# Optimization experiments

Hardware: AMD Instinct MI355X
Metric: run time of the kernel (lower is better)

## Reference

```python
import jax, jax.numpy as jnp
import numpy as np

HID = 128
OUT = 128
NC = 100000
NA = 1024
FC = 256
FA = 4096

def _sage(x_src, x_dst, ei, Wl, bl, Wr):
    # PyG SAGEConv, mean aggregation, bipartite:
    # out[i] = lin_l(mean_{j->i} x_src[j]) + lin_r(x_dst[i])
    n_dst = x_dst.shape[0]
    src, dst = ei[0], ei[1]
    msg = x_src[src]                                  # [E, F_src] gather
    agg = jax.ops.segment_sum(msg, dst, num_segments=n_dst)
    cnt = jax.ops.segment_sum(jnp.ones((ei.shape[1],), x_src.dtype), dst, num_segments=n_dst)
    mean = agg / jnp.clip(cnt, 1.0, None)[:, None]
    return mean @ Wl.T + bl + x_dst @ Wr.T

def setup_inputs() -> dict:
    key = jax.random.key(0)
    ks = jax.random.split(key, 20)
    d = {}
    d["article_x"] = jax.random.normal(ks[0], (1, FA), jnp.float32)
    d["community_x"] = jax.random.normal(ks[1], (NC, FC), jnp.float32)
    # bipartite edges: row = article node idx (<NA), col = community idx (<NC)
    d["e_wb"] = jnp.stack([jax.random.randint(ks[2], (500000,), 0, NA, jnp.int32),
                            jax.random.randint(ks[3], (500000,), 0, NC, jnp.int32)])
    d["e_mb"] = jnp.stack([jax.random.randint(ks[4], (500000,), 0, NA, jnp.int32),
                            jax.random.randint(ks[5], (500000,), 0, NC, jnp.int32)])
    d["e_cc"] = jax.random.randint(ks[6], (2, 800000), 0, NC, jnp.int32)
    s = lambda k, sh: jax.random.normal(k, sh, jnp.float32) * (1.0 / np.sqrt(sh[-1]))
    d["W_lin1"] = s(ks[7], (NA, FA)); d["b_lin1"] = jnp.zeros((NA,), jnp.float32)
    d["Wl1"] = s(ks[8], (HID, 1));   d["bl1"] = jnp.zeros((HID,), jnp.float32); d["Wr1"] = s(ks[9], (HID, FC))
    d["Wl2"] = s(ks[10], (HID, 1));  d["bl2"] = jnp.zeros((HID,), jnp.float32); d["Wr2"] = s(ks[11], (HID, HID))
    d["Wl3"] = s(ks[12], (HID, HID)); d["bl3"] = jnp.zeros((HID,), jnp.float32); d["Wr3"] = s(ks[13], (HID, FC))
    d["W_lin2"] = s(ks[14], (OUT, HID)); d["b_lin2"] = jnp.zeros((OUT,), jnp.float32)
    d["Wd1"] = s(ks[15], (OUT, 2 * OUT)); d["bd1"] = jnp.zeros((OUT,), jnp.float32)
    d["Wd2"] = s(ks[16], (1, OUT)); d["bd2"] = jnp.zeros((1,), jnp.float32)
    return d

def reference(article_x, community_x, e_wb, e_mb, e_cc,
              W_lin1, b_lin1, Wl1, bl1, Wr1, Wl2, bl2, Wr2,
              Wl3, bl3, Wr3, W_lin2, b_lin2, Wd1, bd1, Wd2, bd2):
    # encoder
    art = (article_x @ W_lin1.T + b_lin1).reshape(NA, 1)      # [1024, 1]
    h1 = jax.nn.relu(_sage(art, community_x, e_wb, Wl1, bl1, Wr1))   # [NC, HID]
    h2 = jax.nn.relu(_sage(art, h1, e_mb, Wl2, bl2, Wr2))            # [NC, HID]
    h3 = jax.nn.relu(_sage(h2, community_x, e_cc, Wl3, bl3, Wr3))    # [NC, HID]
    z = h3 @ W_lin2.T + b_lin2                                       # [NC, OUT]
    # edge decoder on interacts_with edges
    row, col = e_cc[0], e_cc[1]
    zz = jnp.concatenate([z[row], z[col]], axis=-1)                  # [E, 2*OUT]
    h = jax.nn.relu(zz @ Wd1.T + bd1)
    return (h @ Wd2.T + bd2).reshape(-1)                             # [E]
```

## Files before the change

kernel.cpp:

```cpp
#include <hip/hip_runtime.h>

#define NC 100000
#define NA 1024
#define FA 4096
#define NREP 8

typedef _Float16 half8 __attribute__((ext_vector_type(8)));
typedef _Float16 half4v __attribute__((ext_vector_type(4)));
typedef _Float16 half2v __attribute__((ext_vector_type(2)));
typedef float floatx4 __attribute__((ext_vector_type(4)));

#define CNT_OFF 4294967296.0
#define CNT_INV 2.3283064365386963e-10

__device__ __forceinline__ void cvt_range(const float* __restrict__ in,
                                          _Float16* __restrict__ out, int n4,
                                          int bid, int nb) {
    int t = bid * 256 + threadIdx.x;
    int stride = nb * 256;
    for (int i = t; i < n4; i += stride) {
        float4 v = ((const float4*)in)[i];
        half4v h = {(_Float16)v.x, (_Float16)v.y, (_Float16)v.z, (_Float16)v.w};
        ((half4v*)out)[i] = h;
    }
}

__device__ __forceinline__ void edge_seg(const int* __restrict__ ei, int E,
                                         const float* __restrict__ art,
                                         double* __restrict__ acd, int bid, int nb) {
    int t = bid * 256 + threadIdx.x;
    int stride = nb * 256;
    for (int e = t; e < E; e += stride) {
        int s = ei[e], d = ei[E + e];
        atomicAdd(&acd[d], (double)art[s] + CNT_OFF);
    }
}

__device__ __forceinline__ void hist_seg(const int* __restrict__ ei, int E,
                                         int* __restrict__ deg, int bid, int nb) {
    int t = bid * 256 + threadIdx.x;
    int stride = nb * 256;
    for (int e = t; e < E; e += stride) atomicAdd(&deg[ei[E + e]], 1);
}

__device__ __forceinline__ void wcomb_seg(const float* __restrict__ Wd1,
                                          const float* __restrict__ Wlin2,
                                          _Float16* __restrict__ Wuh,
                                          _Float16* __restrict__ Wvh, int bid) {
    int i = bid * 2 + (threadIdx.x >> 7);
    int j = threadIdx.x & 127;
    float au = 0.f, av = 0.f;
    for (int m = 0; m < 128; ++m) {
        float wl = Wlin2[m * 128 + j];
        au = fmaf(Wd1[i * 256 + m], wl, au);
        av = fmaf(Wd1[i * 256 + 128 + m], wl, av);
    }
    Wuh[i * 128 + j] = (_Float16)au;
    Wvh[i * 128 + j] = (_Float16)av;
}

__device__ __forceinline__ void bcomb_seg(const float* __restrict__ Wd1,
                                          const float* __restrict__ b2,
                                          const float* __restrict__ bd1,
                                          float* __restrict__ bu, float* __restrict__ bv) {
    int i = threadIdx.x;
    if (i >= 128) return;
    float su = 0.f, sv = 0.f;
    for (int m = 0; m < 128; ++m) {
        float b = b2[m];
        su = fmaf(Wd1[i * 256 + m], b, su);
        sv = fmaf(Wd1[i * 256 + 128 + m], b, sv);
    }
    bu[i] = su + bd1[i];
    bv[i] = sv;
}

__global__ void k_art(const float* __restrict__ ax, const float* __restrict__ W,
                      const float* __restrict__ b, float* __restrict__ art) {
    int wave = (blockIdx.x * blockDim.x + threadIdx.x) >> 6;
    int lane = threadIdx.x & 63;
    if (wave >= NA) return;
    const float* wr = W + (size_t)wave * FA;
    float s = 0.f;
    #pragma unroll
    for (int i = 0; i < FA; i += 256) {
        float4 a  = *(const float4*)&ax[i + 4 * lane];
        float4 wv = *(const float4*)&wr[i + 4 * lane];
        s += a.x * wv.x + a.y * wv.y + a.z * wv.z + a.w * wv.w;
    }
    for (int off = 32; off; off >>= 1) s += __shfl_down(s, off);
    if (lane == 0) art[wave] = s + b[wave];
}

#define FRONT_WB   1024
#define FRONT_MB   1024
#define FRONT_HIST 768
#define FRONT_WCVT 96
#define FRONT_WCOMB 64
#define FRONT_BCOMB 1
#define FRONT_CVT  8192
#define FRONT_TOTAL (FRONT_WB + FRONT_MB + FRONT_HIST + FRONT_WCVT + FRONT_WCOMB + FRONT_BCOMB + FRONT_CVT)

__global__ __launch_bounds__(256)
void k_front(const int* __restrict__ e_wb, int E1,
             const int* __restrict__ e_mb, int E2,
             const int* __restrict__ e_cc, int E3,
             const float* __restrict__ art,
             double* __restrict__ acdr1, double* __restrict__ acdr2,
             int* __restrict__ degr,
             const float* __restrict__ Wr1, _Float16* __restrict__ Wr1h,
             const float* __restrict__ Wr2, _Float16* __restrict__ Wr2h,
             const float* __restrict__ Wl3, _Float16* __restrict__ Wl3h,
             const float* __restrict__ Wr3, _Float16* __restrict__ Wr3h,
             const float* __restrict__ Wd1, const float* __restrict__ Wlin2,
             _Float16* __restrict__ Wuh, _Float16* __restrict__ Wvh,
             const float* __restrict__ b2, const float* __restrict__ bd1,
             float* __restrict__ bu, float* __restrict__ bv,
             const float* __restrict__ cx, _Float16* __restrict__ cxh)
{
    int b = blockIdx.x;
    if (b < FRONT_WB) { edge_seg(e_wb, E1, art, acdr1 + (size_t)(b & (NREP-1)) * NC, b, FRONT_WB); return; }
    b -= FRONT_WB;
    if (b < FRONT_MB) { edge_seg(e_mb, E2, art, acdr2 + (size_t)(b & (NREP-1)) * NC, b, FRONT_MB); return; }
    b -= FRONT_MB;
    if (b < FRONT_HIST) { hist_seg(e_cc, E3, degr + (size_t)(b & (NREP-1)) * NC, b, FRONT_HIST); return; }
    b -= FRONT_HIST;
    if (b < FRONT_WCVT) {
        if (b < 32) cvt_range(Wr1, Wr1h, 8192, b, 32);
        else if (b < 48) cvt_range(Wr2, Wr2h, 4096, b - 32, 16);
        else if (b < 64) cvt_range(Wl3, Wl3h, 4096, b - 48, 16);
        else cvt_range(Wr3, Wr3h, 8192, b - 64, 32);
        return;
    }
    b -= FRONT_WCVT;
    if (b < FRONT_WCOMB) { wcomb_seg(Wd1, Wlin2, Wuh, Wvh, b); return; }
    b -= FRONT_WCOMB;
    if (b < FRONT_BCOMB) { bcomb_seg(Wd1, b2, bd1, bu, bv); return; }
    b -= FRONT_BCOMB;
    cvt_range(cx, cxh, NC * 64, b, FRONT_CVT);
}

#define S1R_SCAN 98
#define S1R_RED  ((2 * NC + 255) / 256)
#define S1R_TOTAL (S1R_SCAN + S1R_RED)

__global__ __launch_bounds__(256)
void k_scan1red(const int* __restrict__ degr, int* __restrict__ deg,
                int* __restrict__ pre, int* __restrict__ blksum,
                const double* __restrict__ acdr1, double* __restrict__ acd1,
                const double* __restrict__ acdr2, double* __restrict__ acd2)
{
    if (blockIdx.x >= S1R_SCAN) {
        int i = (blockIdx.x - S1R_SCAN) * 256 + threadIdx.x;
        if (i < NC) {
            double s = 0.0;
            #pragma unroll
            for (int r = 0; r < NREP; ++r) s += acdr1[(size_t)r * NC + i];
            acd1[i] = s;
        } else {
            int j = i - NC;
            if (j < NC) {
                double s = 0.0;
                #pragma unroll
                for (int r = 0; r < NREP; ++r) s += acdr2[(size_t)r * NC + j];
                acd2[j] = s;
            }
        }
        return;
    }
    __shared__ int ts[256];
    int base = blockIdx.x * 1024 + threadIdx.x * 4;
    int v0 = 0, v1 = 0, v2 = 0, v3 = 0;
    #pragma unroll
    for (int r = 0; r < NREP; ++r) {
        const int* dr = degr + (size_t)r * NC;
        if (base + 0 < NC) v0 += dr[base + 0];
        if (base + 1 < NC) v1 += dr[base + 1];
        if (base + 2 < NC) v2 += dr[base + 2];
        if (base + 3 < NC) v3 += dr[base + 3];
    }
    if (base + 0 < NC) deg[base + 0] = v0;
    if (base + 1 < NC) deg[base + 1] = v1;
    if (base + 2 < NC) deg[base + 2] = v2;
    if (base + 3 < NC) deg[base + 3] = v3;
    int tsum = v0 + v1 + v2 + v3;
    ts[threadIdx.x] = tsum;
    __syncthreads();
    for (int off = 1; off < 256; off <<= 1) {
        int y = (threadIdx.x >= off) ? ts[threadIdx.x - off] : 0;
        __syncthreads();
        ts[threadIdx.x] += y;
        __syncthreads();
    }
    int excl = ts[threadIdx.x] - tsum;
    if (base + 0 < NC) pre[base + 0] = excl;
    if (base + 1 < NC) pre[base + 1] = excl + v0;
    if (base + 2 < NC) pre[base + 2] = excl + v0 + v1;
    if (base + 3 < NC) pre[base + 3] = excl + v0 + v1 + v2;
    if (threadIdx.x == 255) blksum[blockIdx.x] = ts[255];
}

__global__ void k_scan2(int* __restrict__ blksum, int NB) {
    __shared__ int ts[256];
    int v = (threadIdx.x < NB) ? blksum[threadIdx.x] : 0;
    ts[threadIdx.x] = v;
    __syncthreads();
    for (int off = 1; off < 256; off <<= 1) {
        int y = (threadIdx.x >= off) ? ts[threadIdx.x - off] : 0;
        __syncthreads();
        ts[threadIdx.x] += y;
        __syncthreads();
    }
    if (threadIdx.x < NB) blksum[threadIdx.x] = ts[threadIdx.x] - v;
}

__global__ void k_scan3(const int* __restrict__ pre, const int* __restrict__ blksum,
                        const int* __restrict__ deg, int* __restrict__ off,
                        int* __restrict__ cursor, float* __restrict__ cntf) {
    int i = blockIdx.x * blockDim.x + threadIdx.x;
    if (i < NC) {
        int o = pre[i] + blksum[i >> 10];
        off[i] = o;
        cursor[i] = o;
        cntf[i] = (float)deg[i];
    }
}

__device__ __forceinline__ float mean_from_packed(double t) {
    double cd = rint(t * CNT_INV);
    float sum = (float)(t - cd * CNT_OFF);
    float cc = (float)cd;
    cc = cc > 1.f ? cc : 1.f;
    return sum / cc;
}

__device__ __forceinline__
void enc12_body(_Float16* lds, int blk,
                const _Float16* __restrict__ cxh, const _Float16* __restrict__ Wr1h,
                const _Float16* __restrict__ Wr2h,
                const float* __restrict__ bl1, const double* __restrict__ acd1,
                const float* __restrict__ Wl1,
                const float* __restrict__ bl2, const double* __restrict__ acd2,
                const float* __restrict__ Wl2,
                _Float16* __restrict__ out, int N)
{
    _Float16* Bh  = lds;
    _Float16* Ah  = lds + 128 * 40;
    _Float16* h1t = lds + 128 * 40;

    const int t = threadIdx.x, lane = t & 63, w = t >> 6;
    const int rowbase = blk * 128;
    const bool isA = t < 128;
    const int rr = isA ? t : t - 128;
    const int fr = lane & 15;
    const int kq = (lane >> 4) << 3;

    floatx4 zero4 = {0.f, 0.f, 0.f, 0.f};
    floatx4 acc[2][8];
    #pragma unroll
    for (int i = 0; i < 2; ++i)
        #pragma unroll
        for (int cf = 0; cf < 8; ++cf) acc[i][cf] = zero4;

    float4 p0, p1, p2, p3;
    float4 zf = make_float4(0.f, 0.f, 0.f, 0.f);
    {
        bool ok = true; const _Float16* base;
        if (isA) { int row = rowbase + rr; ok = row < N; base = ok ? &cxh[(size_t)row * 256] : Ah; }
        else base = &Wr1h[(size_t)rr * 256];
        const float4* s4 = (const float4*)base;
        p0 = ok ? s4[0] : zf; p1 = ok ? s4[1] : zf; p2 = ok ? s4[2] : zf; p3 = ok ? s4[3] : zf;
    }
    for (int tile = 0; tile < 8; ++tile) {
        float4* dst = (float4*)(isA ? &Ah[rr * 40] : &Bh[rr * 40]);
        dst[0] = p0; dst[1] = p1; dst[2] = p2; dst[3] = p3;
        __syncthreads();
        if (tile < 7) {
            int ko = (tile + 1) << 5;
            bool ok = true; const _Float16* base;
            if (isA) { int row = rowbase + rr; ok = row < N; base = ok ? &cxh[(size_t)row * 256 + ko] : Ah; }
            else base = &Wr1h[(size_t)rr * 256 + ko];
            const float4* s4 = (const float4*)base;
            p0 = ok ? s4[0] : zf; p1 = ok ? s4[1] : zf; p2 = ok ? s4[2] : zf; p3 = ok ? s4[3] : zf;
        }
        half8 af0 = *(const half8*)&Ah[(w * 32 + fr) * 40 + kq];
        half8 af1 = *(const half8*)&Ah[(w * 32 + 16 + fr) * 40 + kq];
        #pragma unroll
        for (int cf = 0; cf < 8; ++cf) {
            half8 bf = *(const half8*)&Bh[(cf * 16 + fr) * 40 + kq];
            acc[0][cf] = __builtin_amdgcn_mfma_f32_16x16x32_f16(af0, bf, acc[0][cf], 0, 0, 0);
            acc[1][cf] = __builtin_amdgcn_mfma_f32_16x16x32_f16(af1, bf, acc[1][cf], 0, 0, 0);
        }
        __syncthreads();
    }

    {
        float blc[8], wlc[8];
        #pragma unroll
        for (int cf = 0; cf < 8; ++cf) { int col = cf * 16 + fr; blc[cf] = bl1[col]; wlc[cf] = Wl1[col]; }
        #pragma unroll
        for (int i = 0; i < 2; ++i) {
            #pragma unroll
            for (int j = 0; j < 4; ++j) {
                int lrow = w * 32 + i * 16 + ((lane >> 4) << 2) + j;
                int grow = rowbase + lrow;
                float m = 0.f;
                if (grow < N) m = mean_from_packed(acd1[grow]);
                #pragma unroll
                for (int cf = 0; cf < 8; ++cf) {
                    float v = acc[i][cf][j] + blc[cf] + m * wlc[cf];
                    v = fmaxf(v, 0.f);
                    h1t[lrow * 136 + cf * 16 + fr] = (_Float16)v;
                }
            }
        }
    }
    __syncthreads();

    #pragma unroll
    for (int i = 0; i < 2; ++i)
        #pragma unroll
        for (int cf = 0; cf < 8; ++cf) acc[i][cf] = zero4;
    if (!isA) {
        const float4* s4 = (const float4*)&Wr2h[(size_t)rr * 128];
        p0 = s4[0]; p1 = s4[1]; p2 = s4[2]; p3 = s4[3];
    }
    for (int tt = 0; tt < 4; ++tt) {
        if (!isA) { float4* d = (float4*)&Bh[rr * 40]; d[0] = p0; d[1] = p1; d[2] = p2; d[3] = p3; }
        __syncthreads();
        if (!isA && tt < 3) {
            const float4* s4 = (const float4*)&Wr2h[(size_t)rr * 128 + ((tt + 1) << 5)];
            p0 = s4[0]; p1 = s4[1]; p2 = s4[2]; p3 = s4[3];
        }
        half8 af0 = *(const half8*)&h1t[(w * 32 + fr) * 136 + (tt << 5) + kq];
        half8 af1 = *(const half8*)&h1t[(w * 32 + 16 + fr) * 136 + (tt << 5) + kq];
        #pragma unroll
        for (int cf = 0; cf < 8; ++cf) {
            half8 bf = *(const half8*)&Bh[(cf * 16 + fr) * 40 + kq];
            acc[0][cf] = __builtin_amdgcn_mfma_f32_16x16x32_f16(af0, bf, acc[0][cf], 0, 0, 0);
            acc[1][cf] = __builtin_amdgcn_mfma_f32_16x16x32_f16(af1, bf, acc[1][cf], 0, 0, 0);
        }
        __syncthreads();
    }

    {
        float blc[8], wlc[8];
        #pragma unroll
        for (int cf = 0; cf < 8; ++cf) { int col = cf * 16 + fr; blc[cf] = bl2[col]; wlc[cf] = Wl2[col]; }
        #pragma unroll
        for (int i = 0; i < 2; ++i) {
            #pragma unroll
            for (int j = 0; j < 4; ++j) {
                int grow = rowbase + w * 32 + i * 16 + ((lane >> 4) << 2) + j;
                if (grow < N) {
                    float m = mean_from_packed(acd2[grow]);
                    #pragma unroll
                    for (int cf = 0; cf < 8; ++cf) {
                        float v = acc[i][cf][j] + blc[cf] + m * wlc[cf];
                        v = fmaxf(v, 0.f);
                        out[(size_t)grow * 128 + cf * 16 + fr] = (_Float16)v;
                    }
                }
            }
        }
    }
}

#define MID_SC  256
#define MID_GB  ((NC + 127) / 128)

__global__ __launch_bounds__(256)
void k_mid(const _Float16* __restrict__ cxh, const _Float16* __restrict__ Wr1h,
           const _Float16* __restrict__ Wr2h,
           const float* __restrict__ bl1, const double* __restrict__ acd1,
           const float* __restrict__ Wl1,
           const float* __restrict__ bl2, const double* __restrict__ acd2,
           const float* __restrict__ Wl2,
           _Float16* __restrict__ out, int N,
           const int* __restrict__ e_cc, int E3,
           int* __restrict__ cursor, int2* __restrict__ se)
{
    __shared__ _Float16 lds[128 * 40 + 128 * 136];
    if (blockIdx.x < MID_SC) {
        int t = blockIdx.x * 256 + threadIdx.x;
        int stride = MID_SC * 256;
        #pragma unroll 4
        for (int e = t; e < E3; e += stride) {
            int s = e_cc[e], d = e_cc[E3 + e];
            int p = atomicAdd(&cursor[d], 1);
            se[p] = make_int2(s, e);
        }
        return;
    }
    enc12_body(lds, blockIdx.x - MID_SC, cxh, Wr1h, Wr2h, bl1, acd1, Wl1, bl2, acd2, Wl2, out, N);
}

__global__ __launch_bounds__(256)
void k_csr_agg_h(const int* __restrict__ off, const int* __restrict__ deg,
                 const int2* __restrict__ se, const _Float16* __restrict__ h,
                 _Float16* __restrict__ agg) {
    int node = (blockIdx.x * blockDim.x + threadIdx.x) >> 6;
    int lane = threadIdx.x & 63;
    if (node >= NC) return;
    int b = off[node], d = deg[node];
    int dm = d < 64 ? d : 64;
    int sj = 0;
    if (lane < dm) sj = se[b + lane].x;
    float sx = 0.f, sy = 0.f;
    #pragma unroll 4
    for (int j = 0; j < dm; ++j) {
        int src = __shfl(sj, j);
        half2v m = *(const half2v*)&h[(size_t)src * 128 + 2 * lane];
        sx += (float)m[0]; sy += (float)m[1];
    }
    for (int j = 64; j < d; ++j) {
        int src = se[b + j].x;
        half2v m = *(const half2v*)&h[(size_t)src * 128 + 2 * lane];
        sx += (float)m[0]; sy += (float)m[1];
    }
    half2v r = {(_Float16)sx, (_Float16)sy};
    *(half2v*)&agg[(size_t)node * 128 + 2 * lane] = r;
}

__global__ __launch_bounds__(256)
void k_enc3uv(const _Float16* __restrict__ aggh, const _Float16* __restrict__ Wl3h,
              const _Float16* __restrict__ cxh, const _Float16* __restrict__ Wr3h,
              const float* __restrict__ bl3, const float* __restrict__ rcnt,
              const _Float16* __restrict__ Wuh, const float* __restrict__ bu,
              const _Float16* __restrict__ Wvh, const float* __restrict__ bv,
              _Float16* __restrict__ uout, _Float16* __restrict__ vout, int N)
{
    __shared__ _Float16 lds[128 * 40 + 128 * 136];
    _Float16* Bh  = lds;
    _Float16* Ah  = lds + 128 * 40;
    _Float16* h3t = lds + 128 * 40;

    const int t = threadIdx.x, lane = t & 63, w = t >> 6;
    const int rowbase = blockIdx.x * 128;
    const bool isA = t < 128;
    const int rr = isA ? t : t - 128;
    const int fr = lane & 15;
    const int kq = (lane >> 4) << 3;

    floatx4 zero4 = {0.f, 0.f, 0.f, 0.f};
    floatx4 acc[2][8];
    #pragma unroll
    for (int i = 0; i < 2; ++i)
        #pragma unroll
        for (int cf = 0; cf < 8; ++cf) acc[i][cf] = zero4;

    float4 p0, p1, p2, p3;
    float4 zf = make_float4(0.f, 0.f, 0.f, 0.f);
    {
        bool ok = true; const _Float16* base;
        if (isA) { int row = rowbase + rr; ok = row < N; base = ok ? &aggh[(size_t)row * 128] : Ah; }
        else base = &Wl3h[(size_t)rr * 128];
        const float4* s4 = (const float4*)base;
        p0 = ok ? s4[0] : zf; p1 = ok ? s4[1] : zf; p2 = ok ? s4[2] : zf; p3 = ok ? s4[3] : zf;
    }
    for (int tile = 0; tile < 12; ++tile) {
        float4* dst = (float4*)(isA ? &Ah[rr * 40] : &Bh[rr * 40]);
        dst[0] = p0; dst[1] = p1; dst[2] = p2; dst[3] = p3;
        __syncthreads();
        if (tile < 11) {
            int tn = tile + 1;
            bool ok = true; const _Float16* base;
            if (tn < 4) {
                int ko = tn << 5;
                if (isA) { int row = rowbase + rr; ok = row < N; base = ok ? &aggh[(size_t)row * 128 + ko] : Ah; }
                else base = &Wl3h[(size_t)rr * 128 + ko];
            } else {
                int ko = (tn - 4) << 5;
                if (isA) { int row = rowbase + rr; ok = row < N; base = ok ? &cxh[(size_t)row * 256 + ko] : Ah; }
                else base = &Wr3h[(size_t)rr * 256 + ko];
            }
            const float4* s4 = (const float4*)base;
            p0 = ok ? s4[0] : zf; p1 = ok ? s4[1] : zf; p2 = ok ? s4[2] : zf; p3 = ok ? s4[3] : zf;
        }
        half8 af0 = *(const half8*)&Ah[(w * 32 + fr) * 40 + kq];
        half8 af1 = *(const half8*)&Ah[(w * 32 + 16 + fr) * 40 + kq];
        #pragma unroll
        for (int cf = 0; cf < 8; ++cf) {
            half8 bf = *(const half8*)&Bh[(cf * 16 + fr) * 40 + kq];
            acc[0][cf] = __builtin_amdgcn_mfma_f32_16x16x32_f16(af0, bf, acc[0][cf], 0, 0, 0);
            acc[1][cf] = __builtin_amdgcn_mfma_f32_16x16x32_f16(af1, bf, acc[1][cf], 0, 0, 0);
        }
        if (tile == 3) {
            #pragma unroll
            for (int i = 0; i < 2; ++i)
                #pragma unroll
                for (int j = 0; j < 4; ++j) {
                    int row = rowbase + w * 32 + i * 16 + ((lane >> 4) << 2) + j;
                    float c = (row < N) ? rcnt[row] : 1.f;
                    c = c > 1.f ? c : 1.f;
                    float inv = 1.f / c;
                    #pragma unroll
                    for (int cf = 0; cf < 8; ++cf) acc[i][cf][j] *= inv;
                }
        }
        __syncthreads();
    }

    {
        float blc[8];
        #pragma unroll
        for (int cf = 0; cf < 8; ++cf) blc[cf] = bl3[cf * 16 + fr];
        #pragma unroll
        for (int i = 0; i < 2; ++i) {
            #pragma unroll
            for (int j = 0; j < 4; ++j) {
                int lrow = w * 32 + i * 16 + ((lane >> 4) << 2) + j;
                #pragma unroll
                for (int cf = 0; cf < 8; ++cf) {
                    float v = acc[i][cf][j] + blc[cf];
                    v = fmaxf(v, 0.f);
                    h3t[lrow * 136 + cf * 16 + fr] = (_Float16)v;
                }
            }
        }
    }
    __syncthreads();

    for (int ph = 0; ph < 2; ++ph) {
        const _Float16* Wp = ph ? Wvh : Wuh;
        const float* bp = ph ? bv : bu;
        _Float16* op = ph ? vout : uout;
        #pragma unroll
        for (int i = 0; i < 2; ++i)
            #pragma unroll
            for (int cf = 0; cf < 8; ++cf) acc[i][cf] = zero4;
        if (!isA) {
            const float4* s4 = (const float4*)&Wp[(size_t)rr * 128];
            p0 = s4[0]; p1 = s4[1]; p2 = s4[2]; p3 = s4[3];
        }
        for (int tt = 0; tt < 4; ++tt) {
            if (!isA) { float4* d = (float4*)&Bh[rr * 40]; d[0] = p0; d[1] = p1; d[2] = p2; d[3] = p3; }
            __syncthreads();
            if (!isA && tt < 3) {
                const float4* s4 = (const float4*)&Wp[(size_t)rr * 128 + ((tt + 1) << 5)];
                p0 = s4[0]; p1 = s4[1]; p2 = s4[2]; p3 = s4[3];
            }
            half8 af0 = *(const half8*)&h3t[(w * 32 + fr) * 136 + (tt << 5) + kq];
            half8 af1 = *(const half8*)&h3t[(w * 32 + 16 + fr) * 136 + (tt << 5) + kq];
            #pragma unroll
            for (int cf = 0; cf < 8; ++cf) {
                half8 bf = *(const half8*)&Bh[(cf * 16 + fr) * 40 + kq];
                acc[0][cf] = __builtin_amdgcn_mfma_f32_16x16x32_f16(af0, bf, acc[0][cf], 0, 0, 0);
                acc[1][cf] = __builtin_amdgcn_mfma_f32_16x16x32_f16(af1, bf, acc[1][cf], 0, 0, 0);
            }
            __syncthreads();
        }
        float bc[8];
        #pragma unroll
        for (int cf = 0; cf < 8; ++cf) bc[cf] = bp[cf * 16 + fr];
        #pragma unroll
        for (int i = 0; i < 2; ++i) {
            #pragma unroll
            for (int j = 0; j < 4; ++j) {
                int grow = rowbase + w * 32 + i * 16 + ((lane >> 4) << 2) + j;
                if (grow < N) {
                    #pragma unroll
                    for (int cf = 0; cf < 8; ++cf)
                        op[(size_t)grow * 128 + cf * 16 + fr] = (_Float16)(acc[i][cf][j] + bc[cf]);
                }
            }
        }
    }
}

__global__ __launch_bounds__(256)
void k_decoder_h(const int* __restrict__ off, const int* __restrict__ deg,
                 const int2* __restrict__ se,
                 const _Float16* __restrict__ u, const _Float16* __restrict__ v,
                 const float* __restrict__ wd2, const float* __restrict__ bd2,
                 float* __restrict__ out) {
    int node = (blockIdx.x * blockDim.x + threadIdx.x) >> 6;
    if (node >= NC) return;
    int lane = threadIdx.x & 63;
    int g = lane >> 3, s = lane & 7;

    float wf[16], vf[16];
    #pragma unroll
    for (int q = 0; q < 16; ++q) wf[q] = wd2[s * 16 + q];
    {
        half8 va = *(const half8*)&v[(size_t)node * 128 + s * 16];
        half8 vb = *(const half8*)&v[(size_t)node * 128 + s * 16 + 8];
        #pragma unroll
        for (int q = 0; q < 8; ++q) { vf[q] = (float)va[q]; vf[8 + q] = (float)vb[q]; }
    }
    float bb = bd2[0];

    int b = off[node], d = deg[node];
    int dm = d < 64 ? d : 64;
    int sj = 0, ej = 0;
    if (lane < dm) { int2 p = se[b + lane]; sj = p.x; ej = p.y; }

    for (int jb = 0; jb < d; jb += 8) {
        int j = jb + g;
        float p = 0.f;
        int eid = 0;
        bool act = j < d;
        int src = 0;
        if (jb < 64) {
            src = __shfl(sj, j);
            eid = __shfl(ej, j);
        } else if (act) {
            int2 pr = se[b + j];
            src = pr.x; eid = pr.y;
        }
        if (act) {
            half8 ua = *(const half8*)&u[(size_t)src * 128 + s * 16];
            half8 ub = *(const half8*)&u[(size_t)src * 128 + s * 16 + 8];
            #pragma unroll
            for (int q = 0; q < 8; ++q) {
                p = fmaf(wf[q],     fmaxf((float)ua[q] + vf[q],     0.f), p);
                p = fmaf(wf[8 + q], fmaxf((float)ub[q] + vf[8 + q], 0.f), p);
            }
        }
        p += __shfl_xor(p, 1);
        p += __shfl_xor(p, 2);
        p += __shfl_xor(p, 4);
        if (act && s == 0) out[eid] = p + bb;
    }
}

extern "C" void kernel_launch(void* const* d_in, const int* in_sizes, int n_in,
                              void* d_out, int out_size, void* d_ws, size_t ws_size,
                              hipStream_t stream) {
    const float* article_x = (const float*)d_in[0];
    const float* cx     = (const float*)d_in[1];
    const int*   e_wb   = (const int*)d_in[2];
    const int*   e_mb   = (const int*)d_in[3];
    const int*   e_cc   = (const int*)d_in[4];
    const float* W_lin1 = (const float*)d_in[5];
    const float* b_lin1 = (const float*)d_in[6];
    const float* Wl1    = (const float*)d_in[7];
    const float* bl1    = (const float*)d_in[8];
    const float* Wr1    = (const float*)d_in[9];
    const float* Wl2    = (const float*)d_in[10];
    const float* bl2    = (const float*)d_in[11];
    const float* Wr2    = (const float*)d_in[12];
    const float* Wl3    = (const float*)d_in[13];
    const float* bl3    = (const float*)d_in[14];
    const float* Wr3    = (const float*)d_in[15];
    const float* W_lin2 = (const float*)d_in[16];
    const float* b_lin2 = (const float*)d_in[17];
    const float* Wd1    = (const float*)d_in[18];
    const float* bd1    = (const float*)d_in[19];
    const float* Wd2    = (const float*)d_in[20];
    const float* bd2    = (const float*)d_in[21];
    float* out = (float*)d_out;

    const int E1 = in_sizes[2] / 2;
    const int E2 = in_sizes[3] / 2;
    const int E3 = in_sizes[4] / 2;

    double* acd1 = (double*)d_ws;
    double* acd2 = acd1 + NC;
    float* ws = (float*)(acd2 + NC);
    size_t o = 0;
    float* art   = ws;      o += 1024;
    float* cnt3f = ws + o;  o += NC;
    float* buf   = ws + o;  o += 128;
    float* bvf   = ws + o;  o += 128;
    int* deg    = (int*)(ws + o); o += NC;
    int* pre    = (int*)(ws + o); o += NC;
    int* off    = (int*)(ws + o); o += NC;
    int* cursor = (int*)(ws + o); o += NC;
    int* blksum = (int*)(ws + o); o += 256;
    int2* se    = (int2*)(ws + o); o += 2 * 800000;
    _Float16* hws = (_Float16*)(ws + o);
    size_t ho = 0;
    _Float16* cxh    = hws + ho; ho += (size_t)NC * 256;
    _Float16* B1h    = hws + ho; ho += (size_t)NC * 128;
    _Float16* B2h    = hws + ho; ho += (size_t)NC * 128;
    _Float16* Wr1h   = hws + ho; ho += 128 * 256;
    _Float16* Wr2h   = hws + ho; ho += 128 * 128;
    _Float16* Wl3h   = hws + ho; ho += 128 * 128;
    _Float16* Wr3h   = hws + ho; ho += 128 * 256;
    _Float16* Wuh    = hws + ho; ho += 128 * 128;
    _Float16* Wvh    = hws + ho; ho += 128 * 128;

    double* acdr1 = (double*)B1h;
    double* acdr2 = acdr1 + (size_t)NREP * NC;
    int*    degr  = (int*)B2h;

    hipMemsetAsync(acdr1, 0, (size_t)2 * NREP * NC * sizeof(double), stream);
    hipMemsetAsync(degr, 0, (size_t)NREP * NC * sizeof(int), stream);

    k_art<<<256, 256, 0, stream>>>(article_x, W_lin1, b_lin1, art);

    k_front<<<FRONT_TOTAL, 256, 0, stream>>>(
        e_wb, E1, e_mb, E2, e_cc, E3, art, acdr1, acdr2, degr,
        Wr1, Wr1h, Wr2, Wr2h, Wl3, Wl3h, Wr3, Wr3h,
        Wd1, W_lin2, Wuh, Wvh, b_lin2, bd1, buf, bvf, cx, cxh);

    k_scan1red<<<S1R_TOTAL, 256, 0, stream>>>(degr, deg, pre, blksum,
                                              acdr1, acd1, acdr2, acd2);
    k_scan2<<<1, 256, 0, stream>>>(blksum, S1R_SCAN);
    k_scan3<<<(NC + 255) / 256, 256, 0, stream>>>(pre, blksum, deg, off, cursor, cnt3f);

    k_mid<<<MID_SC + MID_GB, 256, 0, stream>>>(
        cxh, Wr1h, Wr2h, bl1, acd1, Wl1, bl2, acd2, Wl2,
        B1h, NC, e_cc, E3, cursor, se);

    const int GW = (NC * 64 + 255) / 256;
    k_csr_agg_h<<<GW, 256, 0, stream>>>(off, deg, se, B1h, B2h);
    k_enc3uv<<<MID_GB, 256, 0, stream>>>(B2h, Wl3h, cxh, Wr3h,
                                         bl3, cnt3f, Wuh, buf, Wvh, bvf,
                                         B1h, B2h, NC);
    k_decoder_h<<<GW, 256, 0, stream>>>(off, deg, se, B1h, B2h, Wd2, bd2, out);
}
```

Baseline: 359.2 us.

## Replace global atomics with LDS-partitioned aggregation, histogram, and CSR scatter

Splits destination nodes into 32 ranges that fit in shared memory. Each block scans its 1/16 slice of the edges and accumulates sums, counts and degrees only for its range, using LDS atomics instead of global double and int atomics. Per-slice base offsets are then computed so the CSR scatter also uses LDS cursors. This removes the memsets and global atomic contention, but every block now rereads its whole edge slice, which multiplies edge-index traffic by the number of partitions.

```diff
diff --git a/kernel.cpp b/kernel.cpp
--- a/kernel.cpp
+++ b/kernel.cpp
@@ -3,15 +3,14 @@
 #define NC 100000
 #define NA 1024
 #define FA 4096
-#define NREP 8
+#define PART 32
+#define RANGE 3125
+#define PR 16
 
 typedef _Float16 half8 __attribute__((ext_vector_type(8)));
 typedef _Float16 half4v __attribute__((ext_vector_type(4)));
 typedef _Float16 half2v __attribute__((ext_vector_type(2)));
 typedef float floatx4 __attribute__((ext_vector_type(4)));
-
-#define CNT_OFF 4294967296.0
-#define CNT_INV 2.3283064365386963e-10
 
 __device__ __forceinline__ void cvt_range(const float* __restrict__ in,
                                           _Float16* __restrict__ out, int n4,
@@ -25,22 +24,71 @@
     }
 }
 
-__device__ __forceinline__ void edge_seg(const int* __restrict__ ei, int E,
+__device__ __forceinline__ void agg_part(const int* __restrict__ ei, int E,
                                          const float* __restrict__ art,
-                                         double* __restrict__ acd, int bid, int nb) {
-    int t = bid * 256 + threadIdx.x;
-    int stride = nb * 256;
-    for (int e = t; e < E; e += stride) {
-        int s = ei[e], d = ei[E + e];
-        atomicAdd(&acd[d], (double)art[s] + CNT_OFF);
-    }
-}
-
-__device__ __forceinline__ void hist_seg(const int* __restrict__ ei, int E,
-                                         int* __restrict__ deg, int bid, int nb) {
-    int t = bid * 256 + threadIdx.x;
-    int stride = nb * 256;
-    for (int e = t; e < E; e += stride) atomicAdd(&deg[ei[E + e]], 1);
+                                         float2* __restrict__ acwr,
+                                         float2* lds, int bid) {
+    int p = bid & (PART - 1), r = bid >> 5;
+    int plo = p * RANGE;
+    for (int i = threadIdx.x; i < RANGE; i += 256) lds[i] = make_float2(0.f, 0.f);
+    __syncthreads();
+    int chunk = (E + PR - 1) / PR;
+    int e0 = r * chunk;
+    int e1 = e0 + chunk; if (e1 > E) e1 = E;
+    for (int e = e0 + threadIdx.x; e < e1; e += 256) {
+        int d = ei[E + e];
+        unsigned du = (unsigned)(d - plo);
+        if (du < (unsigned)RANGE) {
+            float a = art[ei[e]];
+            atomicAdd(&lds[du].x, a);
+            atomicAdd(&lds[du].y, 1.f);
+        }
+    }
+    __syncthreads();
+    float2* dst = acwr + (size_t)r * NC + plo;
+    for (int i = threadIdx.x; i < RANGE; i += 256) dst[i] = lds[i];
+}
+
+__device__ __forceinline__ void hist_part(const int* __restrict__ ei, int E,
+                                          int* __restrict__ degr,
+                                          int* lds, int bid) {
+    int p = bid & (PART - 1), r = bid >> 5;
+    int plo = p * RANGE;
+    for (int i = threadIdx.x; i < RANGE; i += 256) lds[i] = 0;
+    __syncthreads();
+    int chunk = (E + PR - 1) / PR;
+    int e0 = r * chunk;
+    int e1 = e0 + chunk; if (e1 > E) e1 = E;
+    for (int e = e0 + threadIdx.x; e < e1; e += 256) {
+        int d = ei[E + e];
+        unsigned du = (unsigned)(d - plo);
+        if (du < (unsigned)RANGE) atomicAdd(&lds[du], 1);
+    }
+    __syncthreads();
+    int* dst = degr + (size_t)r * NC + plo;
+    for (int i = threadIdx.x; i < RANGE; i += 256) dst[i] = lds[i];
+}
+
+__device__ __forceinline__ void scatter_part(const int* __restrict__ ei, int E,
+                                             const int* __restrict__ baseR,
+                                             int2* __restrict__ se,
+                                             int* ldscur, int bid) {
+    int p = bid & (PART - 1), r = bid >> 5;
+    int plo = p * RANGE;
+    const int* bsrc = baseR + (size_t)r * NC + plo;
+    for (int i = threadIdx.x; i < RANGE; i += 256) ldscur[i] = bsrc[i];
+    __syncthreads();
+    int chunk = (E + PR - 1) / PR;
+    int e0 = r * chunk;
+    int e1 = e0 + chunk; if (e1 > E) e1 = E;
+    for (int e = e0 + threadIdx.x; e < e1; e += 256) {
+        int d = ei[E + e];
+        unsigned du = (unsigned)(d - plo);
+        if (du < (unsigned)RANGE) {
+            int pos = atomicAdd(&ldscur[du], 1);
+            se[pos] = make_int2(ei[e], e);
+        }
+    }
 }
 
 __device__ __forceinline__ void wcomb_seg(const float* __restrict__ Wd1,
@@ -92,9 +140,9 @@
     if (lane == 0) art[wave] = s + b[wave];
 }
 
-#define FRONT_WB   1024
-#define FRONT_MB   1024
-#define FRONT_HIST 768
+#define FRONT_WB   (PART * PR)
+#define FRONT_MB   (PART * PR)
+#define FRONT_HIST (PART * PR)
 #define FRONT_WCVT 96
 #define FRONT_WCOMB 64
 #define FRONT_BCOMB 1
@@ -106,7 +154,7 @@
              const int* __restrict__ e_mb, int E2,
              const int* __restrict__ e_cc, int E3,
              const float* __restrict__ art,
-             double* __restrict__ acdr1, double* __restrict__ acdr2,
+             float2* __restrict__ acwr1, float2* __restrict__ acwr2,
              int* __restrict__ degr,
              const float* __restrict__ Wr1, _Float16* __restrict__ Wr1h,
              const float* __restrict__ Wr2, _Float16* __restrict__ Wr2h,
@@ -118,12 +166,13 @@
              float* __restrict__ bu, float* __restrict__ bv,
              const float* __restrict__ cx, _Float16* __restrict__ cxh)
 {
+    __shared__ float2 slds[RANGE];
     int b = blockIdx.x;
-    if (b < FRONT_WB) { edge_seg(e_wb, E1, art, acdr1 + (size_t)(b & (NREP-1)) * NC, b, FRONT_WB); return; }
+    if (b < FRONT_WB) { agg_part(e_wb, E1, art, acwr1, slds, b); return; }
     b -= FRONT_WB;
-    if (b < FRONT_MB) { edge_seg(e_mb, E2, art, acdr2 + (size_t)(b & (NREP-1)) * NC, b, FRONT_MB); return; }
+    if (b < FRONT_MB) { agg_part(e_mb, E2, art, acwr2, slds, b); return; }
     b -= FRONT_MB;
-    if (b < FRONT_HIST) { hist_seg(e_cc, E3, degr + (size_t)(b & (NREP-1)) * NC, b, FRONT_HIST); return; }
+    if (b < FRONT_HIST) { hist_part(e_cc, E3, degr, (int*)slds, b); return; }
     b -= FRONT_HIST;
     if (b < FRONT_WCVT) {
         if (b < 32) cvt_range(Wr1, Wr1h, 8192, b, 32);
@@ -141,30 +190,26 @@
 }
 
 #define S1R_SCAN 98
-#define S1R_RED  ((2 * NC + 255) / 256)
+#define S1R_RED  ((NC + 255) / 256)
 #define S1R_TOTAL (S1R_SCAN + S1R_RED)
 
 __global__ __launch_bounds__(256)
 void k_scan1red(const int* __restrict__ degr, int* __restrict__ deg,
                 int* __restrict__ pre, int* __restrict__ blksum,
-                const double* __restrict__ acdr1, double* __restrict__ acd1,
-                const double* __restrict__ acdr2, double* __restrict__ acd2)
+                const float2* __restrict__ acwr1, float* __restrict__ mean1,
+                const float2* __restrict__ acwr2, float* __restrict__ mean2)
 {
     if (blockIdx.x >= S1R_SCAN) {
         int i = (blockIdx.x - S1R_SCAN) * 256 + threadIdx.x;
         if (i < NC) {
-            double s = 0.0;
-            #pragma unroll
-            for (int r = 0; r < NREP; ++r) s += acdr1[(size_t)r * NC + i];
-            acd1[i] = s;
-        } else {
-            int j = i - NC;
-            if (j < NC) {
-                double s = 0.0;
-                #pragma unroll
-                for (int r = 0; r < NREP; ++r) s += acdr2[(size_t)r * NC + j];
-                acd2[j] = s;
-            }
+            float s1 = 0.f, c1 = 0.f, s2 = 0.f, c2 = 0.f;
+            #pragma unroll
+            for (int r = 0; r < PR; ++r) {
+                float2 v = acwr1[(size_t)r * NC + i]; s1 += v.x; c1 += v.y;
+                float2 w = acwr2[(size_t)r * NC + i]; s2 += w.x; c2 += w.y;
+            }
+            mean1[i] = s1 / fmaxf(c1, 1.f);
+            mean2[i] = s2 / fmaxf(c2, 1.f);
         }
         return;
     }
@@ -172,7 +217,7 @@
     int base = blockIdx.x * 1024 + threadIdx.x * 4;
     int v0 = 0, v1 = 0, v2 = 0, v3 = 0;
     #pragma unroll
-    for (int r = 0; r < NREP; ++r) {
+    for (int r = 0; r < PR; ++r) {
         const int* dr = degr + (size_t)r * NC;
         if (base + 0 < NC) v0 += dr[base + 0];
         if (base + 1 < NC) v1 += dr[base + 1];
@@ -215,32 +260,30 @@
 }
 
 __global__ void k_scan3(const int* __restrict__ pre, const int* __restrict__ blksum,
-                        const int* __restrict__ deg, int* __restrict__ off,
-                        int* __restrict__ cursor, float* __restrict__ cntf) {
+                        const int* __restrict__ degr, const int* __restrict__ deg,
+                        int* __restrict__ off, int* __restrict__ baseR,
+                        float* __restrict__ cntf) {
     int i = blockIdx.x * blockDim.x + threadIdx.x;
     if (i < NC) {
         int o = pre[i] + blksum[i >> 10];
         off[i] = o;
-        cursor[i] = o;
         cntf[i] = (float)deg[i];
-    }
-}
-
-__device__ __forceinline__ float mean_from_packed(double t) {
-    double cd = rint(t * CNT_INV);
-    float sum = (float)(t - cd * CNT_OFF);
-    float cc = (float)cd;
-    cc = cc > 1.f ? cc : 1.f;
-    return sum / cc;
+        int b = o;
+        #pragma unroll
+        for (int r = 0; r < PR; ++r) {
+            baseR[(size_t)r * NC + i] = b;
+            b += degr[(size_t)r * NC + i];
+        }
+    }
 }
 
 __device__ __forceinline__
 void enc12_body(_Float16* lds, int blk,
                 const _Float16* __restrict__ cxh, const _Float16* __restrict__ Wr1h,
                 const _Float16* __restrict__ Wr2h,
-                const float* __restrict__ bl1, const double* __restrict__ acd1,
+                const float* __restrict__ bl1, const float* __restrict__ mean1,
                 const float* __restrict__ Wl1,
-                const float* __restrict__ bl2, const double* __restrict__ acd2,
+                const float* __restrict__ bl2, const float* __restrict__ mean2,
                 const float* __restrict__ Wl2,
                 _Float16* __restrict__ out, int N)
 {
@@ -304,8 +347,7 @@
             for (int j = 0; j < 4; ++j) {
                 int lrow = w * 32 + i * 16 + ((lane >> 4) << 2) + j;
                 int grow = rowbase + lrow;
-                float m = 0.f;
-                if (grow < N) m = mean_from_packed(acd1[grow]);
+                float m = (grow < N) ? mean1[grow] : 0.f;
                 #pragma unroll
                 for (int cf = 0; cf < 8; ++cf) {
                     float v = acc[i][cf][j] + blc[cf] + m * wlc[cf];
@@ -353,7 +395,7 @@
             for (int j = 0; j < 4; ++j) {
                 int grow = rowbase + w * 32 + i * 16 + ((lane >> 4) << 2) + j;
                 if (grow < N) {
-                    float m = mean_from_packed(acd2[grow]);
+                    float m = mean2[grow];
                     #pragma unroll
                     for (int cf = 0; cf < 8; ++cf) {
                         float v = acc[i][cf][j] + blc[cf] + m * wlc[cf];
@@ -366,33 +408,26 @@
     }
 }
 
-#define MID_SC  256
+#define MID_SC  (PART * PR)
 #define MID_GB  ((NC + 127) / 128)
 
 __global__ __launch_bounds__(256)
 void k_mid(const _Float16* __restrict__ cxh, const _Float16* __restrict__ Wr1h,
            const _Float16* __restrict__ Wr2h,
-           const float* __restrict__ bl1, const double* __restrict__ acd1,
+           const float* __restrict__ bl1, const float* __restrict__ mean1,
            const float* __restrict__ Wl1,
-           const float* __restrict__ bl2, const double* __restrict__ acd2,
+           const float* __restrict__ bl2, const float* __restrict__ mean2,
            const float* __restrict__ Wl2,
            _Float16* __restrict__ out, int N,
            const int* __restrict__ e_cc, int E3,
-           int* __restrict__ cursor, int2* __restrict__ se)
+           const int* __restrict__ baseR, int2* __restrict__ se)
 {
     __shared__ _Float16 lds[128 * 40 + 128 * 136];
     if (blockIdx.x < MID_SC) {
-        int t = blockIdx.x * 256 + threadIdx.x;
-        int stride = MID_SC * 256;
-        #pragma unroll 4
-        for (int e = t; e < E3; e += stride) {
-            int s = e_cc[e], d = e_cc[E3 + e];
-            int p = atomicAdd(&cursor[d], 1);
-            se[p] = make_int2(s, e);
-        }
+        scatter_part(e_cc, E3, baseR, se, (int*)lds, blockIdx.x);
         return;
     }
-    enc12_body(lds, blockIdx.x - MID_SC, cxh, Wr1h, Wr2h, bl1, acd1, Wl1, bl2, acd2, Wl2, out, N);
+    enc12_body(lds, blockIdx.x - MID_SC, cxh, Wr1h, Wr2h, bl1, mean1, Wl1, bl2, mean2, Wl2, out, N);
 }
 
 __global__ __launch_bounds__(256)
@@ -655,19 +690,19 @@
     const int E2 = in_sizes[3] / 2;
     const int E3 = in_sizes[4] / 2;
 
-    double* acd1 = (double*)d_ws;
-    double* acd2 = acd1 + NC;
-    float* ws = (float*)(acd2 + NC);
+    float* ws = (float*)d_ws;
     size_t o = 0;
-    float* art   = ws;      o += 1024;
-    float* cnt3f = ws + o;  o += NC;
-    float* buf   = ws + o;  o += 128;
-    float* bvf   = ws + o;  o += 128;
+    float* art    = ws;     o += 1024;
+    float* cnt3f  = ws + o; o += NC;
+    float* mean1f = ws + o; o += NC;
+    float* mean2f = ws + o; o += NC;
+    float* buf    = ws + o; o += 128;
+    float* bvf    = ws + o; o += 128;
     int* deg    = (int*)(ws + o); o += NC;
     int* pre    = (int*)(ws + o); o += NC;
     int* off    = (int*)(ws + o); o += NC;
-    int* cursor = (int*)(ws + o); o += NC;
     int* blksum = (int*)(ws + o); o += 256;
+    int* baseR  = (int*)(ws + o); o += (size_t)PR * NC;
     int2* se    = (int2*)(ws + o); o += 2 * 800000;
     _Float16* hws = (_Float16*)(ws + o);
     size_t ho = 0;
@@ -681,28 +716,25 @@
     _Float16* Wuh    = hws + ho; ho += 128 * 128;
     _Float16* Wvh    = hws + ho; ho += 128 * 128;
 
-    double* acdr1 = (double*)B1h;
-    double* acdr2 = acdr1 + (size_t)NREP * NC;
+    float2* acwr1 = (float2*)B1h;
+    float2* acwr2 = acwr1 + (size_t)PR * NC;
     int*    degr  = (int*)B2h;
 
-    hipMemsetAsync(acdr1, 0, (size_t)2 * NREP * NC * sizeof(double), stream);
-    hipMemsetAsync(degr, 0, (size_t)NREP * NC * sizeof(int), stream);
-
     k_art<<<256, 256, 0, stream>>>(article_x, W_lin1, b_lin1, art);
 
     k_front<<<FRONT_TOTAL, 256, 0, stream>>>(
-        e_wb, E1, e_mb, E2, e_cc, E3, art, acdr1, acdr2, degr,
+        e_wb, E1, e_mb, E2, e_cc, E3, art, acwr1, acwr2, degr,
         Wr1, Wr1h, Wr2, Wr2h, Wl3, Wl3h, Wr3, Wr3h,
         Wd1, W_lin2, Wuh, Wvh, b_lin2, bd1, buf, bvf, cx, cxh);
 
     k_scan1red<<<S1R_TOTAL, 256, 0, stream>>>(degr, deg, pre, blksum,
-                                              acdr1, acd1, acdr2, acd2);
+                                              acwr1, mean1f, acwr2, mean2f);
     k_scan2<<<1, 256, 0, stream>>>(blksum, S1R_SCAN);
-    k_scan3<<<(NC + 255) / 256, 256, 0, stream>>>(pre, blksum, deg, off, cursor, cnt3f);
+    k_scan3<<<(NC + 255) / 256, 256, 0, stream>>>(pre, blksum, degr, deg, off, baseR, cnt3f);
 
     k_mid<<<MID_SC + MID_GB, 256, 0, stream>>>(
-        cxh, Wr1h, Wr2h, bl1, acd1, Wl1, bl2, acd2, Wl2,
-        B1h, NC, e_cc, E3, cursor, se);
+        cxh, Wr1h, Wr2h, bl1, mean1f, Wl1, bl2, mean2f, Wl2,
+        B1h, NC, e_cc, E3, baseR, se);
 
     const int GW = (NC * 64 + 255) / 256;
     k_csr_agg_h<<<GW, 256, 0, stream>>>(off, deg, se, B1h, B2h);
```

After: 428.9 us. +19.4%, slower.
